# Optimization experiments

Measured on AMD Instinct MI355X. Metric: run time of the kernel, lower is better.

## Reference

```python
import jax, jax.numpy as jnp
import numpy as np

T, IN, OUT, RANK, GS = 8192, 4096, 4096, 32, 64  # group_size=64 for int4 precision


def setup_inputs() -> dict:
    key = jax.random.key(0)
    k1, k2, k3, k4, k5, k6 = jax.random.split(key, 6)
    x = jax.random.normal(k1, (T, IN), dtype=jnp.float32)
    # unpacked signed int4 weights in [-8, 7]
    qweight = jax.random.randint(k2, (OUT, IN), -8, 8, dtype=jnp.int32)
    # per-group (along in_features), per-output-channel weight scales
    wscales = jax.random.uniform(k3, (IN // GS, OUT), dtype=jnp.float32) * 0.02 + 0.001
    # smoothing factor, kept away from zero
    smooth_factor = jax.random.uniform(k4, (IN,), dtype=jnp.float32) + 0.5
    proj_down = jax.random.normal(k5, (IN, RANK), dtype=jnp.float32) * 0.02
    proj_up = jax.random.normal(k6, (OUT, RANK), dtype=jnp.float32) * 0.02
    return {"x": x, "qweight": qweight, "wscales": wscales,
            "smooth_factor": smooth_factor, "proj_down": proj_down, "proj_up": proj_up}


def reference(x, qweight, wscales, smooth_factor, proj_down, proj_up):
    t, in_f = x.shape
    out_f = qweight.shape[0]
    g = in_f // GS
    # --- act fuse lora: smooth, quantize per (token, group) to int4, lora_down on smoothed x ---
    xs = x / smooth_factor                                  # [T, IN] smoothed activations
    xg = xs.reshape(t, g, GS)
    amax = jnp.max(jnp.abs(xg), axis=-1, keepdims=True)     # per-token per-group absmax
    ascale = amax / 7.0                                     # int4 symmetric range [-8,7], use 7
    ascale = jnp.where(ascale == 0, jnp.ones_like(ascale), ascale)
    q = jnp.clip(jnp.round(xg / ascale), -8.0, 7.0)         # quantized int4 acts (as float)
    xdq = (q * ascale).reshape(t, in_f)                     # dequantized activations
    lora_act = xs @ proj_down                               # [T, RANK]
    # --- w4a4 gemm with per-group weight dequant + fused lora up ---
    wdq = qweight.astype(x.dtype).reshape(out_f, g, GS) * wscales.T[:, :, None]
    wdq = wdq.reshape(out_f, in_f)                          # dequantized weight [OUT, IN]
    main = xdq @ wdq.T                                      # [T, OUT]
    out = main + lora_act @ proj_up.T                       # fused low-rank correction
    return out
```

## Files before the change

kernel.cpp:

```cpp
#include <hip/hip_runtime.h>
#include <stdint.h>


#define T_DIM 8192
#define IN_DIM 4096
#define OUT_DIM 4096
#define RANK 32
#define KP 4160
#define LORA_OFF 4096
#define ZPAD_OFF 4128
#define CHUNK 512
#define NCHUNK 8
#define NT 65

typedef unsigned short u16;
typedef __attribute__((ext_vector_type(8))) short short8;
typedef __attribute__((ext_vector_type(4))) float f32x4;
typedef __attribute__((address_space(1))) const unsigned int gas_u32;
typedef __attribute__((address_space(3))) unsigned int las_u32;

__device__ __forceinline__ u16 f2bf(float f) {
  unsigned u = __float_as_uint(f);
  u += 0x7FFFu + ((u >> 16) & 1u);
  return (u16)(u >> 16);
}

__global__ __launch_bounds__(256) void k_wdq(const int* __restrict__ qw,
                                             const float* __restrict__ wsc,
                                             u16* __restrict__ B) {
  int o = blockIdx.x >> 2;
  int k0 = ((blockIdx.x & 3) * 256 + threadIdx.x) * 4;
  int4 q = *(const int4*)(qw + (size_t)o * IN_DIM + k0);
  float s = wsc[(k0 >> 6) * OUT_DIM + o];
  ushort4 r;
  r.x = f2bf((float)q.x * s);
  r.y = f2bf((float)q.y * s);
  r.z = f2bf((float)q.z * s);
  r.w = f2bf((float)q.w * s);
  *(ushort4*)(B + (size_t)o * KP + k0) = r;
}

__global__ __launch_bounds__(256) void k_wlora(const float* __restrict__ pu,
                                               u16* __restrict__ B) {
  int id = blockIdx.x * 256 + threadIdx.x;
  int o = id >> 6, c = id & 63;
  u16 v = 0;
  if (c < RANK) v = f2bf(pu[o * RANK + c]);
  B[(size_t)o * KP + LORA_OFF + c] = v;
}

__global__ __launch_bounds__(256) void k_prep(const float* __restrict__ pd,
                                              u16* __restrict__ pdT) {
  int id = blockIdx.x * 256 + threadIdx.x;
  int k = id >> 5, r = id & 31;
  pdT[(size_t)r * IN_DIM + k] = f2bf(pd[(size_t)k * RANK + r]);
}

__global__ __launch_bounds__(256) void k_act(const float* __restrict__ x,
                                             const float* __restrict__ smooth,
                                             const u16* __restrict__ pdT,
                                             u16* __restrict__ A) {
  __shared__ u16 sxs[16 * 512];
  __shared__ float sacc[4][16][32];
  int tid = threadIdx.x;
  int wave = tid >> 6, lane = tid & 63;
  int quad = lane >> 4, l16 = lane & 15;
  int t0 = blockIdx.x * 16;
  int row = tid >> 4;
  int seg = tid & 15;
  const float* xrow = x + (size_t)(t0 + row) * IN_DIM;
  u16* arow = A + (size_t)(t0 + row) * KP;

  f32x4 acc0 = {0.f, 0.f, 0.f, 0.f}, acc1 = {0.f, 0.f, 0.f, 0.f};

  for (int it = 0; it < NCHUNK; ++it) {
    int cbase = it * CHUNK;
    int c0 = cbase + seg * 32;
    float xs[32];
#pragma unroll
    for (int j = 0; j < 8; ++j) {
      float4 xv = *(const float4*)(xrow + c0 + j * 4);
      float4 sv = *(const float4*)(smooth + c0 + j * 4);
      xs[j * 4 + 0] = xv.x / sv.x;
      xs[j * 4 + 1] = xv.y / sv.y;
      xs[j * 4 + 2] = xv.z / sv.z;
      xs[j * 4 + 3] = xv.w / sv.w;
    }
    float m = 0.f;
#pragma unroll
    for (int j = 0; j < 32; ++j) m = fmaxf(m, fabsf(xs[j]));
    m = fmaxf(m, __shfl_xor(m, 1));
    float ascale = m / 7.0f;
    if (ascale == 0.0f) ascale = 1.0f;

    __syncthreads();
#pragma unroll
    for (int j = 0; j < 4; ++j) {
      short8 w8, s8;
#pragma unroll
      for (int e = 0; e < 8; ++e) {
        float a = xs[j * 8 + e];
        float q = fminf(7.0f, fmaxf(-8.0f, rintf(a / ascale)));
        w8[e] = (short)f2bf(q * ascale);
        s8[e] = (short)f2bf(a);
      }
      *(short8*)(arow + c0 + j * 8) = w8;
      int c = seg * 4 + j;
      int slot = c ^ (row & 7);
      *(short8*)((char*)sxs + (row * 64 + slot) * 16) = s8;
    }
    __syncthreads();
#pragma unroll
    for (int kk = 0; kk < 4; ++kk) {
      int crel = wave * 16 + kk * 4 + quad;
      int slot = crel ^ (l16 & 7);
      short8 af = *(const short8*)((const char*)sxs + (l16 * 64 + slot) * 16);
      int kg = cbase + wave * 128 + kk * 32 + quad * 8;
      short8 b0 = *(const short8*)(pdT + (size_t)l16 * IN_DIM + kg);
      short8 b1 = *(const short8*)(pdT + (size_t)(16 + l16) * IN_DIM + kg);
      acc0 = __builtin_amdgcn_mfma_f32_16x16x32_bf16(af, b0, acc0, 0, 0, 0);
      acc1 = __builtin_amdgcn_mfma_f32_16x16x32_bf16(af, b1, acc1, 0, 0, 0);
    }
  }
#pragma unroll
  for (int e = 0; e < 4; ++e) {
    sacc[wave][quad * 4 + e][l16] = acc0[e];
    sacc[wave][quad * 4 + e][16 + l16] = acc1[e];
  }
  __syncthreads();
  for (int t = tid; t < 512; t += 256) {
    int r2 = t >> 5, rk = t & 31;
    float s = sacc[0][r2][rk] + sacc[1][r2][rk] + sacc[2][r2][rk] + sacc[3][r2][rk];
    A[(size_t)(t0 + r2) * KP + LORA_OFF + rk] = f2bf(s);
  }
  {
    int r2 = tid >> 4, c2 = (tid & 15) * 2;
    *(unsigned*)(A + (size_t)(t0 + r2) * KP + ZPAD_OFF + c2) = 0u;
  }
}

#define MFMA __builtin_amdgcn_mfma_f32_16x16x32_bf16
#define BAR __builtin_amdgcn_s_barrier

#define STAGE(gbase, sbase, h, ts)                                            \
  do {                                                                        \
    const u16* _s = (gbase) + (size_t)((h)*128 + stg_r) * KP + (ts)*64 + stg_sc * 8; \
    u16* _d = (sbase) + ((h)*128 + stg_r) * 64 + stg_c * 8;                   \
    __builtin_amdgcn_global_load_lds((gas_u32*)(const void*)_s,               \
                                     (las_u32*)(void*)_d, 16, 0, 0);          \
    __builtin_amdgcn_global_load_lds((gas_u32*)(const void*)(_s + (size_t)8 * KP), \
                                     (las_u32*)(void*)(_d + 8 * 64), 16, 0, 0); \
  } while (0)

#define LDA(base, i, kq) \
  (*(const short8*)((base) + ((i)*32 + wr16 + l16) * 64 + (((kq) ^ l7)) * 8))
#define LDB(base, j, kq) \
  (*(const short8*)((base) + ((j)*64 + wc16 + l16) * 64 + (((kq) ^ l7)) * 8))

__global__ __launch_bounds__(512, 2) void k_gemm(const u16* __restrict__ A,
                                                 const u16* __restrict__ B,
                                                 float* __restrict__ C) {
  extern __shared__ __align__(16) u16 lds[];
  const int tid = threadIdx.x;
  const int wave = tid >> 6, lane = tid & 63;
  const int quad = lane >> 4, l16 = lane & 15, l7 = lane & 7;
  const int wr16 = (wave >> 2) << 4;
  const int wc16 = (wave & 3) << 4;
  const int swz = (blockIdx.x & 7) * 64 + (blockIdx.x >> 3);
  const int t0 = (swz >> 4) * 256;
  const int o0 = (swz & 15) * 256;
  const u16* gA = A + (size_t)t0 * KP;
  const u16* gB = B + (size_t)o0 * KP;
  const int stg_r = wave * 16 + (lane >> 3);
  const int stg_c = lane & 7;
  const int stg_sc = stg_c ^ (lane >> 3);

  u16* const sA0 = lds;
  u16* const sB0 = lds + 16384;
  u16* const sA1 = lds + 32768;
  u16* const sB1 = lds + 32768 + 16384;

  f32x4 acc[8][4];
#pragma unroll
  for (int i = 0; i < 8; ++i)
#pragma unroll
    for (int j = 0; j < 4; ++j)
      acc[i][j] = (f32x4){0.f, 0.f, 0.f, 0.f};

  STAGE(gA, sA0, 0, 0);
  STAGE(gB, sB0, 0, 0);
  STAGE(gB, sB0, 1, 0);
  STAGE(gA, sA0, 1, 0);
  STAGE(gA, sA1, 0, 1);
  STAGE(gB, sB1, 0, 1);
  STAGE(gB, sB1, 1, 1);
  asm volatile("s_waitcnt vmcnt(6)" ::: "memory");
  BAR();

  for (int t = 0; t < NT; ++t) {
    const int cur = t & 1, nxt = cur ^ 1;
    int ts1 = t + 1; if (ts1 >= NT) ts1 = NT - 1;
    int ts2 = t + 2; if (ts2 >= NT) ts2 = NT - 1;
    u16* const sAc = cur ? sA1 : sA0;
    u16* const sBc = cur ? sB1 : sB0;
    u16* const sAn = cur ? sA0 : sA1;

    short8 a[4][2], b0[2][2], b1[2][2];

#pragma unroll
    for (int i = 0; i < 4; ++i) {
      a[i][0] = LDA(sAc, i, quad);
      a[i][1] = LDA(sAc, i, 4 + quad);
    }
#pragma unroll
    for (int j = 0; j < 2; ++j) {
      b0[j][0] = LDB(sBc, j, quad);
      b0[j][1] = LDB(sBc, j, 4 + quad);
    }
    STAGE(gA, sAn, 1, ts1);
    BAR();
    __builtin_amdgcn_s_setprio(1);
#pragma unroll
    for (int i = 0; i < 4; ++i)
#pragma unroll
      for (int j = 0; j < 2; ++j) {
        acc[i][j] = MFMA(a[i][0], b0[j][0], acc[i][j], 0, 0, 0);
        acc[i][j] = MFMA(a[i][1], b0[j][1], acc[i][j], 0, 0, 0);
      }
    __builtin_amdgcn_s_setprio(0);
    BAR();

#pragma unroll
    for (int j = 0; j < 2; ++j) {
      b1[j][0] = LDB(sBc, 2 + j, quad);
      b1[j][1] = LDB(sBc, 2 + j, 4 + quad);
    }
    STAGE(gA, sAc, 0, ts2);
    BAR();
    __builtin_amdgcn_s_setprio(1);
#pragma unroll
    for (int i = 0; i < 4; ++i)
#pragma unroll
      for (int j = 0; j < 2; ++j) {
        acc[i][2 + j] = MFMA(a[i][0], b1[j][0], acc[i][2 + j], 0, 0, 0);
        acc[i][2 + j] = MFMA(a[i][1], b1[j][1], acc[i][2 + j], 0, 0, 0);
      }
    __builtin_amdgcn_s_setprio(0);
    BAR();

#pragma unroll
    for (int i = 0; i < 4; ++i) {
      a[i][0] = LDA(sAc, 4 + i, quad);
      a[i][1] = LDA(sAc, 4 + i, 4 + quad);
    }
    STAGE(gB, sBc, 0, ts2);
    BAR();
    __builtin_amdgcn_s_setprio(1);
#pragma unroll
    for (int i = 0; i < 4; ++i)
#pragma unroll
      for (int j = 0; j < 2; ++j) {
        acc[4 + i][j] = MFMA(a[i][0], b0[j][0], acc[4 + i][j], 0, 0, 0);
        acc[4 + i][j] = MFMA(a[i][1], b0[j][1], acc[4 + i][j], 0, 0, 0);
      }
    __builtin_amdgcn_s_setprio(0);
    BAR();

    STAGE(gB, sBc, 1, ts2);
    BAR();
    __builtin_amdgcn_s_setprio(1);
#pragma unroll
    for (int i = 0; i < 4; ++i)
#pragma unroll
      for (int j = 0; j < 2; ++j) {
        acc[4 + i][2 + j] = MFMA(a[i][0], b1[j][0], acc[4 + i][2 + j], 0, 0, 0);
        acc[4 + i][2 + j] = MFMA(a[i][1], b1[j][1], acc[4 + i][2 + j], 0, 0, 0);
      }
    __builtin_amdgcn_s_setprio(0);
    asm volatile("s_waitcnt vmcnt(6)" ::: "memory");
    BAR();
  }

#pragma unroll
  for (int i = 0; i < 8; ++i) {
    const int row = t0 + i * 32 + wr16 + quad * 4;
#pragma unroll
    for (int j = 0; j < 4; ++j) {
      const int col = o0 + j * 64 + wc16 + l16;
#pragma unroll
      for (int e = 0; e < 4; ++e)
        C[(size_t)(row + e) * OUT_DIM + col] = acc[i][j][e];
    }
  }
}

extern "C" void kernel_launch(void* const* d_in, const int* in_sizes, int n_in,
                              void* d_out, int out_size, void* d_ws, size_t ws_size,
                              hipStream_t stream) {
  const float* x      = (const float*)d_in[0];
  const int*   qw     = (const int*)d_in[1];
  const float* wsc    = (const float*)d_in[2];
  const float* smooth = (const float*)d_in[3];
  const float* pd     = (const float*)d_in[4];
  const float* pu     = (const float*)d_in[5];
  float* out = (float*)d_out;

  char* ws = (char*)d_ws;
  u16* A   = (u16*)ws;
  u16* B   = (u16*)(ws + 68157440);
  u16* pdT = (u16*)(ws + 68157440 + 34078720);

  static int attr_set = 0;
  if (!attr_set) {
    hipFuncSetAttribute(reinterpret_cast<const void*>(k_gemm),
                        hipFuncAttributeMaxDynamicSharedMemorySize, 131072);
    attr_set = 1;
  }

  k_wdq  <<<dim3(OUT_DIM * 4), dim3(256), 0, stream>>>(qw, wsc, B);
  k_wlora<<<dim3(OUT_DIM * 64 / 256), dim3(256), 0, stream>>>(pu, B);
  k_prep <<<dim3(IN_DIM * RANK / 256), dim3(256), 0, stream>>>(pd, pdT);
  k_act  <<<dim3(T_DIM / 16), dim3(256), 0, stream>>>(x, smooth, pdT, A);
  k_gemm <<<dim3(512), dim3(512), 131072, stream>>>(A, B, out);
}
```

Before: 522.3 us.

## Switch main GEMM to int8 MFMA with per-group scale application in epilogue

Activations and weights are now stored as packed int8 values (the int4 codes) instead of dequantized bf16. The GEMM runs one i8 MFMA per 64-wide group and rescales each partial sum by the activation and weight group scales in fp32. The LoRA term moves to a separate bf16 MFMA pass after the main loop. This halves operand bytes and uses the higher-throughput int8 MFMA, but adds per-group convert/multiply-add VALU work, uses more LDS (160KB) and rounds the weight scales to bf16.

Measured after the change: 610.6 us. 1.17x slower.

```diff
diff --git a/kernel.cpp b/kernel.cpp
--- a/kernel.cpp
+++ b/kernel.cpp
@@ -6,16 +6,14 @@
 #define IN_DIM 4096
 #define OUT_DIM 4096
 #define RANK 32
-#define KP 4160
-#define LORA_OFF 4096
-#define ZPAD_OFF 4128
 #define CHUNK 512
 #define NCHUNK 8
-#define NT 65
+#define NG 64
 
 typedef unsigned short u16;
 typedef __attribute__((ext_vector_type(8))) short short8;
 typedef __attribute__((ext_vector_type(4))) float f32x4;
+typedef __attribute__((ext_vector_type(4))) int i32x4;
 typedef __attribute__((address_space(1))) const unsigned int gas_u32;
 typedef __attribute__((address_space(3))) unsigned int las_u32;
 
@@ -25,28 +23,26 @@
   return (u16)(u >> 16);
 }
 
+__device__ __forceinline__ f32x4 cvt4(i32x4 v) {
+  f32x4 r;
+  r[0] = (float)v[0]; r[1] = (float)v[1];
+  r[2] = (float)v[2]; r[3] = (float)v[3];
+  return r;
+}
+
 __global__ __launch_bounds__(256) void k_wdq(const int* __restrict__ qw,
-                                             const float* __restrict__ wsc,
-                                             u16* __restrict__ B) {
-  int o = blockIdx.x >> 2;
-  int k0 = ((blockIdx.x & 3) * 256 + threadIdx.x) * 4;
-  int4 q = *(const int4*)(qw + (size_t)o * IN_DIM + k0);
-  float s = wsc[(k0 >> 6) * OUT_DIM + o];
-  ushort4 r;
-  r.x = f2bf((float)q.x * s);
-  r.y = f2bf((float)q.y * s);
-  r.z = f2bf((float)q.z * s);
-  r.w = f2bf((float)q.w * s);
-  *(ushort4*)(B + (size_t)o * KP + k0) = r;
+                                             char* __restrict__ Bq) {
+  int id = blockIdx.x * 256 + threadIdx.x;
+  int4 q = *(const int4*)(qw + (size_t)id * 4);
+  unsigned p = (unsigned)(q.x & 255) | ((unsigned)(q.y & 255) << 8) |
+               ((unsigned)(q.z & 255) << 16) | ((unsigned)(q.w & 255) << 24);
+  ((unsigned*)Bq)[id] = p;
 }
 
 __global__ __launch_bounds__(256) void k_wlora(const float* __restrict__ pu,
-                                               u16* __restrict__ B) {
+                                               u16* __restrict__ BL) {
   int id = blockIdx.x * 256 + threadIdx.x;
-  int o = id >> 6, c = id & 63;
-  u16 v = 0;
-  if (c < RANK) v = f2bf(pu[o * RANK + c]);
-  B[(size_t)o * KP + LORA_OFF + c] = v;
+  BL[id] = f2bf(pu[id]);
 }
 
 __global__ __launch_bounds__(256) void k_prep(const float* __restrict__ pd,
@@ -59,7 +55,9 @@
 __global__ __launch_bounds__(256) void k_act(const float* __restrict__ x,
                                              const float* __restrict__ smooth,
                                              const u16* __restrict__ pdT,
-                                             u16* __restrict__ A) {
+                                             char* __restrict__ Aq,
+                                             u16* __restrict__ AL,
+                                             float* __restrict__ asT) {
   __shared__ u16 sxs[16 * 512];
   __shared__ float sacc[4][16][32];
   int tid = threadIdx.x;
@@ -69,7 +67,7 @@
   int row = tid >> 4;
   int seg = tid & 15;
   const float* xrow = x + (size_t)(t0 + row) * IN_DIM;
-  u16* arow = A + (size_t)(t0 + row) * KP;
+  char* aqrow = Aq + (size_t)(t0 + row) * IN_DIM;
 
   f32x4 acc0 = {0.f, 0.f, 0.f, 0.f}, acc1 = {0.f, 0.f, 0.f, 0.f};
 
@@ -92,19 +90,24 @@
     m = fmaxf(m, __shfl_xor(m, 1));
     float ascale = m / 7.0f;
     if (ascale == 0.0f) ascale = 1.0f;
+    if ((seg & 1) == 0)
+      asT[(size_t)(c0 >> 6) * T_DIM + (t0 + row)] = ascale;
 
     __syncthreads();
 #pragma unroll
     for (int j = 0; j < 4; ++j) {
-      short8 w8, s8;
+      short8 s8;
+      unsigned lo = 0, hi = 0;
 #pragma unroll
       for (int e = 0; e < 8; ++e) {
         float a = xs[j * 8 + e];
-        float q = fminf(7.0f, fmaxf(-8.0f, rintf(a / ascale)));
-        w8[e] = (short)f2bf(q * ascale);
+        float qf = fminf(7.0f, fmaxf(-8.0f, rintf(a / ascale)));
+        int qi = (int)qf;
+        unsigned ub = (unsigned)(qi & 255);
+        if (e < 4) lo |= ub << (8 * e); else hi |= ub << (8 * (e - 4));
         s8[e] = (short)f2bf(a);
       }
-      *(short8*)(arow + c0 + j * 8) = w8;
+      *(uint2*)(aqrow + c0 + j * 8) = make_uint2(lo, hi);
       int c = seg * 4 + j;
       int slot = c ^ (row & 7);
       *(short8*)((char*)sxs + (row * 64 + slot) * 16) = s8;
@@ -131,54 +134,70 @@
   for (int t = tid; t < 512; t += 256) {
     int r2 = t >> 5, rk = t & 31;
     float s = sacc[0][r2][rk] + sacc[1][r2][rk] + sacc[2][r2][rk] + sacc[3][r2][rk];
-    A[(size_t)(t0 + r2) * KP + LORA_OFF + rk] = f2bf(s);
-  }
-  {
-    int r2 = tid >> 4, c2 = (tid & 15) * 2;
-    *(unsigned*)(A + (size_t)(t0 + r2) * KP + ZPAD_OFF + c2) = 0u;
-  }
-}
-
-#define MFMA __builtin_amdgcn_mfma_f32_16x16x32_bf16
+    AL[(size_t)(t0 + r2) * RANK + rk] = f2bf(s);
+  }
+}
+
+#define MFMAI8 __builtin_amdgcn_mfma_i32_16x16x64_i8
+#define MFMABF __builtin_amdgcn_mfma_f32_16x16x32_bf16
 #define BAR __builtin_amdgcn_s_barrier
 
-#define STAGE(gbase, sbase, h, ts)                                            \
+#define STAGEQ(gbase, sbase, h, kt)                                           \
   do {                                                                        \
-    const u16* _s = (gbase) + (size_t)((h)*128 + stg_r) * KP + (ts)*64 + stg_sc * 8; \
-    u16* _d = (sbase) + ((h)*128 + stg_r) * 64 + stg_c * 8;                   \
+    const char* _s = (const char*)(gbase) +                                   \
+        (size_t)((h)*128 + stq_r) * IN_DIM + (size_t)(kt)*64 + stq_cs * 16;   \
+    char* _d = (char*)(sbase) + (h)*8192 + tid * 16;                          \
     __builtin_amdgcn_global_load_lds((gas_u32*)(const void*)_s,               \
                                      (las_u32*)(void*)_d, 16, 0, 0);          \
-    __builtin_amdgcn_global_load_lds((gas_u32*)(const void*)(_s + (size_t)8 * KP), \
-                                     (las_u32*)(void*)(_d + 8 * 64), 16, 0, 0); \
   } while (0)
 
-#define LDA(base, i, kq) \
-  (*(const short8*)((base) + ((i)*32 + wr16 + l16) * 64 + (((kq) ^ l7)) * 8))
-#define LDB(base, j, kq) \
-  (*(const short8*)((base) + ((j)*64 + wc16 + l16) * 64 + (((kq) ^ l7)) * 8))
-
-__global__ __launch_bounds__(512, 2) void k_gemm(const u16* __restrict__ A,
-                                                 const u16* __restrict__ B,
+#define STAGEL(gbase, sbase, h)                                               \
+  do {                                                                        \
+    const char* _s = (const char*)(gbase) +                                   \
+        (size_t)((h)*128 + stq_r) * 64 + stq_cs * 16;                         \
+    char* _d = (char*)(sbase) + (h)*8192 + tid * 16;                          \
+    __builtin_amdgcn_global_load_lds((gas_u32*)(const void*)_s,               \
+                                     (las_u32*)(void*)_d, 16, 0, 0);          \
+  } while (0)
+
+#define LDAQ(base, i) \
+  (*(const i32x4*)((const char*)(base) + ((i)*32 + wr16 + l16) * 64 + ((quad ^ swa) << 4)))
+#define LDBQ(base, j) \
+  (*(const i32x4*)((const char*)(base) + ((j)*64 + wc16 + l16) * 64 + ((quad ^ swb) << 4)))
+#define LDAL(base, i) \
+  (*(const short8*)((const char*)(base) + ((i)*32 + wr16 + l16) * 64 + ((quad ^ swa) << 4)))
+#define LDBL(base, j) \
+  (*(const short8*)((const char*)(base) + ((j)*64 + wc16 + l16) * 64 + ((quad ^ swb) << 4)))
+#define WSLD(g, j) \
+  __uint_as_float((unsigned)sWSp[(g)*256 + (j)*64 + wc16 + l16] << 16)
+
+__global__ __launch_bounds__(512, 2) void k_gemm(const char* __restrict__ Aq,
+                                                 const char* __restrict__ Bq,
+                                                 const u16* __restrict__ AL,
+                                                 const u16* __restrict__ BL,
+                                                 const float* __restrict__ asT,
+                                                 const float* __restrict__ wsc,
                                                  float* __restrict__ C) {
-  extern __shared__ __align__(16) u16 lds[];
+  extern __shared__ __align__(16) char lds[];
   const int tid = threadIdx.x;
   const int wave = tid >> 6, lane = tid & 63;
-  const int quad = lane >> 4, l16 = lane & 15, l7 = lane & 7;
+  const int quad = lane >> 4, l16 = lane & 15;
   const int wr16 = (wave >> 2) << 4;
   const int wc16 = (wave & 3) << 4;
+  const int swa = ((wr16 + l16) ^ ((wr16 + l16) >> 2)) & 3;
+  const int swb = ((wc16 + l16) ^ ((wc16 + l16) >> 2)) & 3;
   const int swz = (blockIdx.x & 7) * 64 + (blockIdx.x >> 3);
   const int t0 = (swz >> 4) * 256;
   const int o0 = (swz & 15) * 256;
-  const u16* gA = A + (size_t)t0 * KP;
-  const u16* gB = B + (size_t)o0 * KP;
-  const int stg_r = wave * 16 + (lane >> 3);
-  const int stg_c = lane & 7;
-  const int stg_sc = stg_c ^ (lane >> 3);
-
-  u16* const sA0 = lds;
-  u16* const sB0 = lds + 16384;
-  u16* const sA1 = lds + 32768;
-  u16* const sB1 = lds + 32768 + 16384;
+  const char* gAq = Aq + (size_t)t0 * IN_DIM;
+  const char* gBq = Bq + (size_t)o0 * IN_DIM;
+  const char* gAL = (const char*)AL + (size_t)t0 * 64;
+  const char* gBL = (const char*)BL + (size_t)o0 * 64;
+  const int stq_r = tid >> 2;
+  const int stq_cs = (tid & 3) ^ ((stq_r ^ (stq_r >> 2)) & 3);
+
+  float* const sASf = (float*)(lds + 65536);
+  u16* const sWSp = (u16*)(lds + 131072);
 
   f32x4 acc[8][4];
 #pragma unroll
@@ -186,99 +205,111 @@
 #pragma unroll
     for (int j = 0; j < 4; ++j)
       acc[i][j] = (f32x4){0.f, 0.f, 0.f, 0.f};
-
-  STAGE(gA, sA0, 0, 0);
-  STAGE(gB, sB0, 0, 0);
-  STAGE(gB, sB0, 1, 0);
-  STAGE(gA, sA0, 1, 0);
-  STAGE(gA, sA1, 0, 1);
-  STAGE(gB, sB1, 0, 1);
-  STAGE(gB, sB1, 1, 1);
-  asm volatile("s_waitcnt vmcnt(6)" ::: "memory");
+  const i32x4 zeroi = {0, 0, 0, 0};
+
+  for (int v = tid; v < 16384; v += 512) {
+    int g = v >> 8, c = v & 255;
+    sWSp[v] = f2bf(wsc[(size_t)g * OUT_DIM + o0 + c]);
+    sASf[v] = asT[(size_t)g * T_DIM + t0 + c];
+  }
+
+  STAGEQ(gAq, lds, 0, 0);           STAGEQ(gAq, lds, 1, 0);
+  STAGEQ(gBq, lds + 16384, 0, 0);   STAGEQ(gBq, lds + 16384, 1, 0);
+  STAGEQ(gAq, lds + 32768, 0, 1);   STAGEQ(gAq, lds + 32768, 1, 1);
+  STAGEQ(gBq, lds + 49152, 0, 1);   STAGEQ(gBq, lds + 49152, 1, 1);
+  asm volatile("s_waitcnt vmcnt(4) lgkmcnt(0)" ::: "memory");
   BAR();
 
-  for (int t = 0; t < NT; ++t) {
-    const int cur = t & 1, nxt = cur ^ 1;
-    int ts1 = t + 1; if (ts1 >= NT) ts1 = NT - 1;
-    int ts2 = t + 2; if (ts2 >= NT) ts2 = NT - 1;
-    u16* const sAc = cur ? sA1 : sA0;
-    u16* const sBc = cur ? sB1 : sB0;
-    u16* const sAn = cur ? sA0 : sA1;
-
-    short8 a[4][2], b0[2][2], b1[2][2];
+  for (int t = 0; t < NG; ++t) {
+    const int cur = t & 1;
+    int ts2 = t + 2; if (ts2 > NG - 1) ts2 = NG - 1;
+    char* const sAc = cur ? lds + 32768 : lds;
+    char* const sBc = cur ? lds + 49152 : lds + 16384;
+    const float* asg = sASf + (size_t)t * 256;
+
+    i32x4 a[4], b0v[2], b1v[2];
+    f32x4 as_lo[4], as_hi[4];
 
 #pragma unroll
     for (int i = 0; i < 4; ++i) {
-      a[i][0] = LDA(sAc, i, quad);
-      a[i][1] = LDA(sAc, i, 4 + quad);
-    }
-#pragma unroll
-    for (int j = 0; j < 2; ++j) {
-      b0[j][0] = LDB(sBc, j, quad);
-      b0[j][1] = LDB(sBc, j, 4 + quad);
-    }
-    STAGE(gA, sAn, 1, ts1);
+      a[i] = LDAQ(sAc, i);
+      as_lo[i] = *(const f32x4*)(asg + i * 32 + wr16 + quad * 4);
+    }
+    b0v[0] = LDBQ(sBc, 0); b0v[1] = LDBQ(sBc, 1);
+    float w0 = WSLD(t, 0), w1 = WSLD(t, 1);
     BAR();
     __builtin_amdgcn_s_setprio(1);
 #pragma unroll
     for (int i = 0; i < 4; ++i)
 #pragma unroll
       for (int j = 0; j < 2; ++j) {
-        acc[i][j] = MFMA(a[i][0], b0[j][0], acc[i][j], 0, 0, 0);
-        acc[i][j] = MFMA(a[i][1], b0[j][1], acc[i][j], 0, 0, 0);
+        i32x4 q4 = MFMAI8(a[i], b0v[j], zeroi, 0, 0, 0);
+        acc[i][j] += cvt4(q4) * (as_lo[i] * (j ? w1 : w0));
       }
     __builtin_amdgcn_s_setprio(0);
     BAR();
 
-#pragma unroll
-    for (int j = 0; j < 2; ++j) {
-      b1[j][0] = LDB(sBc, 2 + j, quad);
-      b1[j][1] = LDB(sBc, 2 + j, 4 + quad);
-    }
-    STAGE(gA, sAc, 0, ts2);
+    b1v[0] = LDBQ(sBc, 2); b1v[1] = LDBQ(sBc, 3);
+    float w2 = WSLD(t, 2), w3 = WSLD(t, 3);
+    STAGEQ(gAq, sAc, 0, ts2);
     BAR();
     __builtin_amdgcn_s_setprio(1);
 #pragma unroll
     for (int i = 0; i < 4; ++i)
 #pragma unroll
       for (int j = 0; j < 2; ++j) {
-        acc[i][2 + j] = MFMA(a[i][0], b1[j][0], acc[i][2 + j], 0, 0, 0);
-        acc[i][2 + j] = MFMA(a[i][1], b1[j][1], acc[i][2 + j], 0, 0, 0);
+        i32x4 q4 = MFMAI8(a[i], b1v[j], zeroi, 0, 0, 0);
+        acc[i][2 + j] += cvt4(q4) * (as_lo[i] * (j ? w3 : w2));
       }
     __builtin_amdgcn_s_setprio(0);
     BAR();
 
 #pragma unroll
     for (int i = 0; i < 4; ++i) {
-      a[i][0] = LDA(sAc, 4 + i, quad);
-      a[i][1] = LDA(sAc, 4 + i, 4 + quad);
-    }
-    STAGE(gB, sBc, 0, ts2);
+      a[i] = LDAQ(sAc, 4 + i);
+      as_hi[i] = *(const f32x4*)(asg + (4 + i) * 32 + wr16 + quad * 4);
+    }
+    STAGEQ(gBq, sBc, 0, ts2);
     BAR();
     __builtin_amdgcn_s_setprio(1);
 #pragma unroll
     for (int i = 0; i < 4; ++i)
 #pragma unroll
       for (int j = 0; j < 2; ++j) {
-        acc[4 + i][j] = MFMA(a[i][0], b0[j][0], acc[4 + i][j], 0, 0, 0);
-        acc[4 + i][j] = MFMA(a[i][1], b0[j][1], acc[4 + i][j], 0, 0, 0);
+        i32x4 q4 = MFMAI8(a[i], b0v[j], zeroi, 0, 0, 0);
+        acc[4 + i][j] += cvt4(q4) * (as_hi[i] * (j ? w1 : w0));
       }
     __builtin_amdgcn_s_setprio(0);
     BAR();
 
-    STAGE(gB, sBc, 1, ts2);
+    STAGEQ(gAq, sAc, 1, ts2);
+    STAGEQ(gBq, sBc, 1, ts2);
     BAR();
     __builtin_amdgcn_s_setprio(1);
 #pragma unroll
     for (int i = 0; i < 4; ++i)
 #pragma unroll
       for (int j = 0; j < 2; ++j) {
-        acc[4 + i][2 + j] = MFMA(a[i][0], b1[j][0], acc[4 + i][2 + j], 0, 0, 0);
-        acc[4 + i][2 + j] = MFMA(a[i][1], b1[j][1], acc[4 + i][2 + j], 0, 0, 0);
+        i32x4 q4 = MFMAI8(a[i], b1v[j], zeroi, 0, 0, 0);
+        acc[4 + i][2 + j] += cvt4(q4) * (as_hi[i] * (j ? w3 : w2));
       }
     __builtin_amdgcn_s_setprio(0);
-    asm volatile("s_waitcnt vmcnt(6)" ::: "memory");
-    BAR();
+    asm volatile("s_waitcnt vmcnt(4)" ::: "memory");
+    BAR();
+  }
+
+  asm volatile("s_waitcnt vmcnt(0)" ::: "memory");
+  BAR();
+  STAGEL(gAL, lds, 0);          STAGEL(gAL, lds, 1);
+  STAGEL(gBL, lds + 16384, 0);  STAGEL(gBL, lds + 16384, 1);
+  asm volatile("s_waitcnt vmcnt(0)" ::: "memory");
+  BAR();
+#pragma unroll
+  for (int i = 0; i < 8; ++i) {
+    short8 al = LDAL(lds, i);
+#pragma unroll
+    for (int j = 0; j < 4; ++j)
+      acc[i][j] = MFMABF(al, LDBL(lds + 16384, j), acc[i][j], 0, 0, 0);
   }
 
 #pragma unroll
@@ -306,20 +337,23 @@
   float* out = (float*)d_out;
 
   char* ws = (char*)d_ws;
-  u16* A   = (u16*)ws;
-  u16* B   = (u16*)(ws + 68157440);
-  u16* pdT = (u16*)(ws + 68157440 + 34078720);
+  char*  Aq  = ws;
+  char*  Bq  = ws + 33554432;
+  u16*   AL  = (u16*)(ws + 50331648);
+  u16*   BL  = (u16*)(ws + 50855936);
+  float* asT = (float*)(ws + 51118080);
+  u16*   pdT = (u16*)(ws + 53215232);
 
   static int attr_set = 0;
   if (!attr_set) {
     hipFuncSetAttribute(reinterpret_cast<const void*>(k_gemm),
-                        hipFuncAttributeMaxDynamicSharedMemorySize, 131072);
+                        hipFuncAttributeMaxDynamicSharedMemorySize, 163840);
     attr_set = 1;
   }
 
-  k_wdq  <<<dim3(OUT_DIM * 4), dim3(256), 0, stream>>>(qw, wsc, B);
-  k_wlora<<<dim3(OUT_DIM * 64 / 256), dim3(256), 0, stream>>>(pu, B);
+  k_wdq  <<<dim3(16384), dim3(256), 0, stream>>>(qw, Bq);
+  k_wlora<<<dim3(512), dim3(256), 0, stream>>>(pu, BL);
   k_prep <<<dim3(IN_DIM * RANK / 256), dim3(256), 0, stream>>>(pd, pdT);
-  k_act  <<<dim3(T_DIM / 16), dim3(256), 0, stream>>>(x, smooth, pdT, A);
-  k_gemm <<<dim3(512), dim3(512), 131072, stream>>>(A, B, out);
-}
+  k_act  <<<dim3(T_DIM / 16), dim3(256), 0, stream>>>(x, smooth, pdT, Aq, AL, asT);
+  k_gemm <<<dim3(512), dim3(512), 163840, stream>>>(Aq, Bq, AL, BL, asT, wsc, out);
+}
```

## Split activation quantize kernel along K with separate lora reduction kernel

Applied to the files above, without the earlier changes.

The activation smoothing/quantization kernel now processes one quarter of the input features per block, launching four times as many blocks. Each block writes a partial lora_down result to a float workspace buffer. A new fixup kernel sums the four partials, writes the bf16 lora columns and zero padding into A. This aims to raise occupancy and memory-level parallelism in the bandwidth-bound activation pass, at the cost of an extra launch and partial-sum traffic.

After: 529.5 us. Within noise of the previous version (+1.4%).

```diff
diff --git a/kernel.cpp b/kernel.cpp
--- a/kernel.cpp
+++ b/kernel.cpp
@@ -10,7 +10,6 @@
 #define LORA_OFF 4096
 #define ZPAD_OFF 4128
 #define CHUNK 512
-#define NCHUNK 8
 #define NT 65
 
 typedef unsigned short u16;
@@ -59,13 +58,16 @@
 __global__ __launch_bounds__(256) void k_act(const float* __restrict__ x,
                                              const float* __restrict__ smooth,
                                              const u16* __restrict__ pdT,
-                                             u16* __restrict__ A) {
+                                             u16* __restrict__ A,
+                                             float* __restrict__ lpart) {
   __shared__ u16 sxs[16 * 512];
   __shared__ float sacc[4][16][32];
   int tid = threadIdx.x;
   int wave = tid >> 6, lane = tid & 63;
   int quad = lane >> 4, l16 = lane & 15;
-  int t0 = blockIdx.x * 16;
+  int tile = blockIdx.x & 511;
+  int slice = blockIdx.x >> 9;
+  int t0 = tile * 16;
   int row = tid >> 4;
   int seg = tid & 15;
   const float* xrow = x + (size_t)(t0 + row) * IN_DIM;
@@ -73,8 +75,8 @@
 
   f32x4 acc0 = {0.f, 0.f, 0.f, 0.f}, acc1 = {0.f, 0.f, 0.f, 0.f};
 
-  for (int it = 0; it < NCHUNK; ++it) {
-    int cbase = it * CHUNK;
+  for (int it = 0; it < 2; ++it) {
+    int cbase = slice * 1024 + it * CHUNK;
     int c0 = cbase + seg * 32;
     float xs[32];
 #pragma unroll
@@ -131,12 +133,20 @@
   for (int t = tid; t < 512; t += 256) {
     int r2 = t >> 5, rk = t & 31;
     float s = sacc[0][r2][rk] + sacc[1][r2][rk] + sacc[2][r2][rk] + sacc[3][r2][rk];
-    A[(size_t)(t0 + r2) * KP + LORA_OFF + rk] = f2bf(s);
-  }
-  {
-    int r2 = tid >> 4, c2 = (tid & 15) * 2;
-    *(unsigned*)(A + (size_t)(t0 + r2) * KP + ZPAD_OFF + c2) = 0u;
-  }
+    lpart[((size_t)slice * T_DIM + (t0 + r2)) * RANK + rk] = s;
+  }
+}
+
+__global__ __launch_bounds__(256) void k_fixup(const float* __restrict__ lpart,
+                                               u16* __restrict__ A) {
+  int id = blockIdx.x * 256 + threadIdx.x;
+  int t = id >> 5, c = id & 31;
+  size_t base = (size_t)t * RANK + c;
+  float s = lpart[base] + lpart[(size_t)T_DIM * RANK + base] +
+            lpart[(size_t)2 * T_DIM * RANK + base] +
+            lpart[(size_t)3 * T_DIM * RANK + base];
+  A[(size_t)t * KP + LORA_OFF + c] = f2bf(s);
+  A[(size_t)t * KP + ZPAD_OFF + c] = 0;
 }
 
 #define MFMA __builtin_amdgcn_mfma_f32_16x16x32_bf16
@@ -198,7 +208,7 @@
   BAR();
 
   for (int t = 0; t < NT; ++t) {
-    const int cur = t & 1, nxt = cur ^ 1;
+    const int cur = t & 1;
     int ts1 = t + 1; if (ts1 >= NT) ts1 = NT - 1;
     int ts2 = t + 2; if (ts2 >= NT) ts2 = NT - 1;
     u16* const sAc = cur ? sA1 : sA0;
@@ -306,9 +316,10 @@
   float* out = (float*)d_out;
 
   char* ws = (char*)d_ws;
-  u16* A   = (u16*)ws;
-  u16* B   = (u16*)(ws + 68157440);
-  u16* pdT = (u16*)(ws + 68157440 + 34078720);
+  u16*   A     = (u16*)ws;
+  u16*   B     = (u16*)(ws + 68157440);
+  u16*   pdT   = (u16*)(ws + 102236160);
+  float* lpart = (float*)(ws + 102498304);
 
   static int attr_set = 0;
   if (!attr_set) {
@@ -320,6 +331,7 @@
   k_wdq  <<<dim3(OUT_DIM * 4), dim3(256), 0, stream>>>(qw, wsc, B);
   k_wlora<<<dim3(OUT_DIM * 64 / 256), dim3(256), 0, stream>>>(pu, B);
   k_prep <<<dim3(IN_DIM * RANK / 256), dim3(256), 0, stream>>>(pd, pdT);
-  k_act  <<<dim3(T_DIM / 16), dim3(256), 0, stream>>>(x, smooth, pdT, A);
+  k_act  <<<dim3(2048), dim3(256), 0, stream>>>(x, smooth, pdT, A, lpart);
+  k_fixup<<<dim3(T_DIM * RANK / 256), dim3(256), 0, stream>>>(lpart, A);
   k_gemm <<<dim3(512), dim3(512), 131072, stream>>>(A, B, out);
 }
```
